# Kernel tuning notes

Measured on AMD Instinct MI355X. Metric: run time of the kernel, lower is better.

Reference implementation:

```python
import jax, jax.numpy as jnp
import numpy as np

N_QUBITS = 24          # must be divisible by 3
DIM = 2 ** N_QUBITS    # 16777216 amplitudes
N_GROUPS = N_QUBITS // 3  # 8 disjoint 3-qubit gate applications


def setup_inputs() -> dict:
    key = jax.random.key(0)
    k1, k2, k3 = jax.random.split(key, 3)
    feature = jax.random.normal(k1, (DIM,), dtype=jnp.float32)
    # Build a random 8x8 unitary as expm of an anti-Hermitian generator,
    # mirroring equivar_gate_matrix = expm(generator) in the original.
    m = (jax.random.normal(k2, (8, 8), dtype=jnp.float32)
         + 1j * jax.random.normal(k3, (8, 8), dtype=jnp.float32)).astype(jnp.complex64)
    gen = 0.5 * (m - m.conj().T)
    gate = jax.scipy.linalg.expm(gen)
    return {
        "feature": feature,
        "gate_real": jnp.real(gate).astype(jnp.float32),
        "gate_imag": jnp.imag(gate).astype(jnp.float32),
    }


def _apply_3q_gate(state, gate, axis):
    # state: (8,)*N_GROUPS complex tensor; contract gate (8x8) into `axis`.
    out = jnp.tensordot(gate, state, axes=[[1], [axis]])  # contracted axis -> front
    return jnp.moveaxis(out, 0, axis)


def reference(feature, gate_real, gate_imag):
    # AmplitudeEmbedding: L2-normalize the feature vector into the state.
    norm = jnp.sqrt(jnp.sum(feature * feature))
    state = (feature / norm).astype(jnp.complex64)
    # View the 24 qubits as 8 groups of 3 (each group = one axis of size 8).
    state = state.reshape((8,) * N_GROUPS)
    gate = (gate_real + 1j * gate_imag).astype(jnp.complex64)
    # QubitUnitary(equivar_gate_matrix, wires=(3i, 3i+1, 3i+2)) for each group.
    for g in range(N_GROUPS):
        state = _apply_3q_gate(state, gate, g)
    # qml.probs(): |amplitude|^2 over the full computational basis.
    probs = (jnp.real(state) ** 2 + jnp.imag(state) ** 2).reshape(-1)
    return probs.astype(jnp.float32)
```

## Files before the change

### kernel.cpp

```cpp
#include <hip/hip_runtime.h>


typedef _Float16 f16;
typedef _Float16 f16x4 __attribute__((ext_vector_type(4)));
typedef float f32x4 __attribute__((ext_vector_type(4)));
typedef unsigned int u32;
typedef unsigned short u16;

__device__ __forceinline__ u32 SW(u32 a) { return a ^ (((a >> 8) & 0xFu) << 3); }

__device__ __forceinline__ u32 PK(float x, float y) {
  return __builtin_bit_cast(u32, __builtin_amdgcn_cvt_pkrtz(x, y));
}

__device__ __forceinline__ f16x4 build_A(const float* __restrict__ gr,
                                         const float* __restrict__ gi, int l) {
  const int row = l & 15, kg = l >> 4;
  const int pg = row & 7, rpl = row >> 3, kpl = kg >> 1;
  f16x4 a;
#pragma unroll
  for (int e = 0; e < 4; ++e) {
    const int j = (kg & 1) * 4 + e;
    const float grv = gr[pg * 8 + j], giv = gi[pg * 8 + j];
    const float v = rpl == 0 ? (kpl == 0 ? grv : -giv) : (kpl == 0 ? giv : grv);
    a[e] = (f16)v;
  }
  return a;
}

__device__ __forceinline__ void lds_stage(char* lb, f16x4 A, int w, int l) {
  const int kg = l >> 4, c = l & 15, c3 = c >> 3, p = kg >> 1;
  const u32 rb = (u32)(w * 512 + c * 32 + kg * 8);
  const f32x4 Z = {0.f, 0.f, 0.f, 0.f};
  f32x4 acc[16];
#pragma unroll
  for (int g = 0; g < 4; ++g) {
#pragma unroll
    for (int m = 0; m < 4; ++m) {
      const int j = (g & 1) + m * 2 + (g >> 1) * 8;
      const uint2 bw = *(const uint2*)(lb + SW(rb + (u32)j * 8192u));
      acc[g * 4 + m] = __builtin_amdgcn_mfma_f32_16x16x16f16(
          A, __builtin_bit_cast(f16x4, bw), Z, 0, 0, 0);
    }
  }
  __syncthreads();
  const u32 wl = (u32)(((w >> 2) << 14) + (((w & 3) * 2 + c3) << 11) +
                       ((c & 7) << 8) + ((kg & 1) << 7) + (p << 4));
#pragma unroll
  for (int g = 0; g < 4; ++g) {
#pragma unroll
    for (int rr = 0; rr < 4; ++rr) {
      const u32 d0 = PK(acc[g * 4 + 0][rr], acc[g * 4 + 1][rr]);
      const u32 d1 = PK(acc[g * 4 + 2][rr], acc[g * 4 + 3][rr]);
      const u32 lg = wl + (u32)(((g & 1) << 16) + ((g >> 1) << 3) + (rr << 5));
      *(uint2*)(lb + SW(lg)) = make_uint2(d0, d1);
    }
  }
  __syncthreads();
}

__global__ __launch_bounds__(1024, 4) void k_pass1(
    const float* __restrict__ f, const float* __restrict__ gr,
    const float* __restrict__ gi, uint4* __restrict__ st,
    float* __restrict__ wsp) {
  __shared__ __align__(16) char lb[131072];
  __shared__ float red[16];
  const int t = threadIdx.x, l = t & 63, w = t >> 6, blk = blockIdx.x;
  const int kg = l >> 4, c = l & 15, c3 = c >> 3, p = kg >> 1;
  const f16x4 A = build_A(gr, gi, l);

  float s = 0.f;
  const float4* fin = (const float4*)f + (size_t)blk * 8192;
  const u32 fl = (u32)(((t >> 7) << 14) + (((t >> 4) & 7) << 11) +
                       (((t >> 1) & 7) << 8) + ((t & 1) << 7));
#pragma unroll
  for (int g2 = 0; g2 < 2; ++g2) {
    float4 v0 = fin[(g2 * 4 + 0) * 1024 + t];
    float4 v1 = fin[(g2 * 4 + 1) * 1024 + t];
    float4 v2 = fin[(g2 * 4 + 2) * 1024 + t];
    float4 v3 = fin[(g2 * 4 + 3) * 1024 + t];
    s += v0.x * v0.x + v0.y * v0.y + v0.z * v0.z + v0.w * v0.w;
    s += v1.x * v1.x + v1.y * v1.y + v1.z * v1.z + v1.w * v1.w;
    s += v2.x * v2.x + v2.y * v2.y + v2.z * v2.z + v2.w * v2.w;
    s += v3.x * v3.x + v3.y * v3.y + v3.z * v3.z + v3.w * v3.w;
#pragma unroll
    for (int q = 0; q < 4; ++q) {
      const float a0 = q == 0 ? v0.x : q == 1 ? v0.y : q == 2 ? v0.z : v0.w;
      const float a1 = q == 0 ? v1.x : q == 1 ? v1.y : q == 2 ? v1.z : v1.w;
      const float a2 = q == 0 ? v2.x : q == 1 ? v2.y : q == 2 ? v2.z : v2.w;
      const float a3 = q == 0 ? v3.x : q == 1 ? v3.y : q == 2 ? v3.z : v3.w;
      const u32 lg = fl + (u32)((q << 5) + (g2 << 3));
      *(uint2*)(lb + SW(lg)) = make_uint2(PK(a0, a1), PK(a2, a3));
      *(uint2*)(lb + SW(lg + 16u)) = make_uint2(0u, 0u);
    }
  }
#pragma unroll
  for (int off = 32; off; off >>= 1) s += __shfl_down(s, off, 64);
  if (l == 0) red[w] = s;
  __syncthreads();
  if (t == 0) {
    float a = 0.f;
#pragma unroll
    for (int i = 0; i < 16; ++i) a += red[i];
    wsp[blk] = a;
  }

  lds_stage(lb, A, w, l);
  lds_stage(lb, A, w, l);
  lds_stage(lb, A, w, l);
  lds_stage(lb, A, w, l);

  const u32 rb = (u32)(w * 512 + c * 32 + kg * 8);
  const f32x4 Z = {0.f, 0.f, 0.f, 0.f};
  const size_t ob = (size_t)blk * 8192;
#pragma unroll
  for (int j = 0; j < 16; ++j) {
    const uint2 bw = *(const uint2*)(lb + SW(rb + (u32)j * 8192u));
    const f32x4 a = __builtin_amdgcn_mfma_f32_16x16x16f16(
        A, __builtin_bit_cast(f16x4, bw), Z, 0, 0, 0);
    const u32 h01 = PK(a[0], a[1]), h23 = PK(a[2], a[3]);
    const u32 q01 = __shfl_xor(h01, 32, 64), q23 = __shfl_xor(h23, 32, 64);
    if (p == 0) {
      const int A3 = j >> 1, A4 = (j & 1) * 4 + (w >> 2), A5 = (w & 3) * 2 + c3;
      uint4 vv;
      vv.x = (h01 & 0xffffu) | (q01 << 16);
      vv.y = (h01 >> 16) | (q01 & 0xffff0000u);
      vv.z = (h23 & 0xffffu) | (q23 << 16);
      vv.w = (h23 >> 16) | (q23 & 0xffff0000u);
      st[ob + (u32)(((A3 * 64 + A4 * 8 + A5) << 4) + ((c & 7) << 1) + (kg & 1))] = vv;
    }
  }
}

__global__ __launch_bounds__(1024, 4) void k_pass2(
    const uint4* gp, const float* __restrict__ gr, const float* __restrict__ gi,
    const float* __restrict__ wsp, float* out) {
  __shared__ __align__(16) char lb[131072];
  __shared__ float red[16];
  const int t = threadIdx.x, l = t & 63, w = t >> 6, b = blockIdx.x;
  const int kg = l >> 4, c = l & 15, c3 = c >> 3, p = kg >> 1;
  const f16x4 A = build_A(gr, gi, l);

  float sp = (t < 512) ? wsp[t] : 0.f;
#pragma unroll
  for (int off = 32; off; off >>= 1) sp += __shfl_down(sp, off, 64);
  if (l == 0) red[w] = sp;

  const u32 fl = (u32)(((t >> 7) << 14) + (((t >> 1) & 7) << 8) +
                       ((t & 1) << 7) + (((t >> 4) & 7) << 1));
#pragma unroll
  for (int it = 0; it < 8; ++it) {
    const uint4 raw = gp[(size_t)(it * 64 + (t >> 4)) * 8192 + (u32)(b * 16 + (t & 15))];
    const u32 lgb = fl + (u32)(it << 11);
#pragma unroll
    for (int dq = 0; dq < 4; ++dq) {
      const u32 dw = dq == 0 ? raw.x : dq == 1 ? raw.y : dq == 2 ? raw.z : raw.w;
      const u32 lg = lgb + (u32)(dq << 5);
      *(u16*)(lb + SW(lg)) = (u16)(dw & 0xffffu);
      *(u16*)(lb + SW(lg + 16u)) = (u16)(dw >> 16);
    }
  }
  __syncthreads();
  float inv;
  {
    float a = 0.f;
#pragma unroll
    for (int i = 0; i < 16; ++i) a += red[i];
    inv = 1.0f / a;
  }

  lds_stage(lb, A, w, l);
  lds_stage(lb, A, w, l);

  const u32 l3 = (u32)((c3 << 14) + ((c & 7) << 11) + ((w & 7) << 5) + (kg << 3));
  const f32x4 Z = {0.f, 0.f, 0.f, 0.f};
#pragma unroll
  for (int j = 0; j < 16; ++j) {
    const u32 jp = (u32)(((j >> 2) << 15) + ((j & 3) << 8) + ((w >> 3) << 10));
    const uint2 bw = *(const uint2*)(lb + SW(l3 + jp));
    const f32x4 a = __builtin_amdgcn_mfma_f32_16x16x16f16(
        A, __builtin_bit_cast(f16x4, bw), Z, 0, 0, 0);
    const int A1 = w & 7, A2 = (w >> 3) * 4 + (j & 3);
    const int A6 = (j >> 2) * 2 + c3, A7 = c & 7;
    const size_t gb = ((size_t)A1 << 18) + ((size_t)A2 << 15) +
                      (u32)(b * 64 + A6 * 8 + A7);
#pragma unroll
    for (int rr = 0; rr < 4; ++rr) {
      float qv = a[rr] * a[rr];
      qv += __shfl_xor(qv, 32, 64);
      if ((rr >> 1) == p) {
        out[gb + ((size_t)((kg & 1) * 4 + rr) << 21)] = qv * inv;
      }
    }
  }
}

extern "C" void kernel_launch(void* const* d_in, const int* in_sizes, int n_in,
                              void* d_out, int out_size, void* d_ws,
                              size_t ws_size, hipStream_t stream) {
  (void)in_sizes; (void)n_in; (void)out_size; (void)ws_size;
  const float* f = (const float*)d_in[0];
  const float* gr = (const float*)d_in[1];
  const float* gi = (const float*)d_in[2];
  float* wsp = (float*)d_ws;

  k_pass1<<<dim3(512), dim3(1024), 0, stream>>>(f, gr, gi, (uint4*)d_out, wsp);
  k_pass2<<<dim3(512), dim3(1024), 0, stream>>>((const uint4*)d_out, gr, gi,
                                                wsp, (float*)d_out);
}
```

Measured before the change: 71.36 us.

## Fuse first gate stage into global load and shrink pass2 blocks

Pass1 now loads the input amplitudes straight from global memory into MFMA B operands, applying the first gate contraction in registers. This drops one LDS staging round trip, so only three LDS stages remain instead of four. Pass2 is restructured into 256-thread blocks with 32KB of LDS, a new swizzle and a new data layout, and the grid grows to 2048 blocks to raise occupancy and overlap. The trade-off is scalar, strided global loads in pass1 in place of float4 loads, which may reduce coalescing.

```diff
diff --git a/kernel.cpp b/kernel.cpp
--- a/kernel.cpp
+++ b/kernel.cpp
@@ -7,7 +7,8 @@
 typedef unsigned int u32;
 typedef unsigned short u16;
 
-__device__ __forceinline__ u32 SW(u32 a) { return a ^ (((a >> 8) & 0xFu) << 3); }
+__device__ __forceinline__ u32 SW1(u32 a) { return a ^ (((a >> 8) & 0xFu) << 3); }
+__device__ __forceinline__ u32 SW2(u32 a) { return a ^ (((a >> 7) & 0x7u) << 4); }
 
 __device__ __forceinline__ u32 PK(float x, float y) {
   return __builtin_bit_cast(u32, __builtin_amdgcn_cvt_pkrtz(x, y));
@@ -28,7 +29,7 @@
   return a;
 }
 
-__device__ __forceinline__ void lds_stage(char* lb, f16x4 A, int w, int l) {
+__device__ __forceinline__ void p1_stage(char* lb, f16x4 A, int w, int l) {
   const int kg = l >> 4, c = l & 15, c3 = c >> 3, p = kg >> 1;
   const u32 rb = (u32)(w * 512 + c * 32 + kg * 8);
   const f32x4 Z = {0.f, 0.f, 0.f, 0.f};
@@ -38,7 +39,7 @@
 #pragma unroll
     for (int m = 0; m < 4; ++m) {
       const int j = (g & 1) + m * 2 + (g >> 1) * 8;
-      const uint2 bw = *(const uint2*)(lb + SW(rb + (u32)j * 8192u));
+      const uint2 bw = *(const uint2*)(lb + SW1(rb + (u32)j * 8192u));
       acc[g * 4 + m] = __builtin_amdgcn_mfma_f32_16x16x16f16(
           A, __builtin_bit_cast(f16x4, bw), Z, 0, 0, 0);
     }
@@ -53,7 +54,7 @@
       const u32 d0 = PK(acc[g * 4 + 0][rr], acc[g * 4 + 1][rr]);
       const u32 d1 = PK(acc[g * 4 + 2][rr], acc[g * 4 + 3][rr]);
       const u32 lg = wl + (u32)(((g & 1) << 16) + ((g >> 1) << 3) + (rr << 5));
-      *(uint2*)(lb + SW(lg)) = make_uint2(d0, d1);
+      *(uint2*)(lb + SW1(lg)) = make_uint2(d0, d1);
     }
   }
   __syncthreads();
@@ -68,30 +69,42 @@
   const int t = threadIdx.x, l = t & 63, w = t >> 6, blk = blockIdx.x;
   const int kg = l >> 4, c = l & 15, c3 = c >> 3, p = kg >> 1;
   const f16x4 A = build_A(gr, gi, l);
+  const f32x4 Z = {0.f, 0.f, 0.f, 0.f};
 
   float s = 0.f;
-  const float4* fin = (const float4*)f + (size_t)blk * 8192;
-  const u32 fl = (u32)(((t >> 7) << 14) + (((t >> 4) & 7) << 11) +
-                       (((t >> 1) & 7) << 8) + ((t & 1) << 7));
-#pragma unroll
-  for (int g2 = 0; g2 < 2; ++g2) {
-    float4 v0 = fin[(g2 * 4 + 0) * 1024 + t];
-    float4 v1 = fin[(g2 * 4 + 1) * 1024 + t];
-    float4 v2 = fin[(g2 * 4 + 2) * 1024 + t];
-    float4 v3 = fin[(g2 * 4 + 3) * 1024 + t];
-    s += v0.x * v0.x + v0.y * v0.y + v0.z * v0.z + v0.w * v0.w;
-    s += v1.x * v1.x + v1.y * v1.y + v1.z * v1.z + v1.w * v1.w;
-    s += v2.x * v2.x + v2.y * v2.y + v2.z * v2.z + v2.w * v2.w;
-    s += v3.x * v3.x + v3.y * v3.y + v3.z * v3.z + v3.w * v3.w;
-#pragma unroll
-    for (int q = 0; q < 4; ++q) {
-      const float a0 = q == 0 ? v0.x : q == 1 ? v0.y : q == 2 ? v0.z : v0.w;
-      const float a1 = q == 0 ? v1.x : q == 1 ? v1.y : q == 2 ? v1.z : v1.w;
-      const float a2 = q == 0 ? v2.x : q == 1 ? v2.y : q == 2 ? v2.z : v2.w;
-      const float a3 = q == 0 ? v3.x : q == 1 ? v3.y : q == 2 ? v3.z : v3.w;
-      const u32 lg = fl + (u32)((q << 5) + (g2 << 3));
-      *(uint2*)(lb + SW(lg)) = make_uint2(PK(a0, a1), PK(a2, a3));
-      *(uint2*)(lb + SW(lg + 16u)) = make_uint2(0u, 0u);
+  {
+    const float* fb = f + ((size_t)blk << 15) + (size_t)(kg & 1) * 16384;
+    f32x4 acc[16];
+#pragma unroll
+    for (int g = 0; g < 4; ++g) {
+#pragma unroll
+      for (int m = 0; m < 4; ++m) {
+        const int j = (g & 1) + m * 2 + (g >> 1) * 8;
+        const int col = (j >> 1) * 512 + (j & 1) * 256 + (w >> 2) * 64 +
+                        (w & 3) * 16 + c;
+        f16x4 b = {(f16)0.f, (f16)0.f, (f16)0.f, (f16)0.f};
+        if (kg < 2) {
+          const float v0 = fb[col];
+          const float v1 = fb[col + 4096];
+          const float v2 = fb[col + 8192];
+          const float v3 = fb[col + 12288];
+          s += v0 * v0 + v1 * v1 + v2 * v2 + v3 * v3;
+          b[0] = (f16)v0; b[1] = (f16)v1; b[2] = (f16)v2; b[3] = (f16)v3;
+        }
+        acc[g * 4 + m] = __builtin_amdgcn_mfma_f32_16x16x16f16(A, b, Z, 0, 0, 0);
+      }
+    }
+    const u32 wl = (u32)(((w >> 2) << 14) + (((w & 3) * 2 + c3) << 11) +
+                         ((c & 7) << 8) + ((kg & 1) << 7) + (p << 4));
+#pragma unroll
+    for (int g = 0; g < 4; ++g) {
+#pragma unroll
+      for (int rr = 0; rr < 4; ++rr) {
+        const u32 d0 = PK(acc[g * 4 + 0][rr], acc[g * 4 + 1][rr]);
+        const u32 d1 = PK(acc[g * 4 + 2][rr], acc[g * 4 + 3][rr]);
+        const u32 lg = wl + (u32)(((g & 1) << 16) + ((g >> 1) << 3) + (rr << 5));
+        *(uint2*)(lb + SW1(lg)) = make_uint2(d0, d1);
+      }
     }
   }
 #pragma unroll
@@ -105,17 +118,15 @@
     wsp[blk] = a;
   }
 
-  lds_stage(lb, A, w, l);
-  lds_stage(lb, A, w, l);
-  lds_stage(lb, A, w, l);
-  lds_stage(lb, A, w, l);
+  p1_stage(lb, A, w, l);
+  p1_stage(lb, A, w, l);
+  p1_stage(lb, A, w, l);
 
   const u32 rb = (u32)(w * 512 + c * 32 + kg * 8);
-  const f32x4 Z = {0.f, 0.f, 0.f, 0.f};
   const size_t ob = (size_t)blk * 8192;
 #pragma unroll
   for (int j = 0; j < 16; ++j) {
-    const uint2 bw = *(const uint2*)(lb + SW(rb + (u32)j * 8192u));
+    const uint2 bw = *(const uint2*)(lb + SW1(rb + (u32)j * 8192u));
     const f32x4 a = __builtin_amdgcn_mfma_f32_16x16x16f16(
         A, __builtin_bit_cast(f16x4, bw), Z, 0, 0, 0);
     const u32 h01 = PK(a[0], a[1]), h23 = PK(a[2], a[3]);
@@ -132,64 +143,101 @@
   }
 }
 
-__global__ __launch_bounds__(1024, 4) void k_pass2(
+__device__ __forceinline__ void p2_stage(char* lb, f16x4 A, int w, int l) {
+  const int kg = l >> 4, c = l & 15, pp = kg >> 1;
+  const f32x4 Z = {0.f, 0.f, 0.f, 0.f};
+  f32x4 acc[16];
+#pragma unroll
+  for (int g = 0; g < 4; ++g) {
+#pragma unroll
+    for (int m = 0; m < 4; ++m) {
+      const int j = (g & 1) + m * 2 + (g >> 1) * 8;
+      const u32 rb = (u32)(j * 2048 + w * 512 + c * 32 + kg * 8);
+      const uint2 bw = *(const uint2*)(lb + SW2(rb));
+      acc[g * 4 + m] = __builtin_amdgcn_mfma_f32_16x16x16f16(
+          A, __builtin_bit_cast(f16x4, bw), Z, 0, 0, 0);
+    }
+  }
+  __syncthreads();
+#pragma unroll
+  for (int pe = 0; pe < 2; ++pe) {
+#pragma unroll
+    for (int rr = 0; rr < 4; ++rr) {
+      uint4 vv;
+      vv.x = PK(acc[pe * 4 + 0][rr], acc[pe * 4 + 1][rr]);
+      vv.y = PK(acc[pe * 4 + 2][rr], acc[pe * 4 + 3][rr]);
+      vv.z = PK(acc[(2 + pe) * 4 + 0][rr], acc[(2 + pe) * 4 + 1][rr]);
+      vv.w = PK(acc[(2 + pe) * 4 + 2][rr], acc[(2 + pe) * 4 + 3][rr]);
+      const u32 wb = (u32)((pe * 4 + w) * 4096 + ((kg & 1) * 4 + rr) * 512 +
+                           c * 32 + pp * 16);
+      *(uint4*)(lb + SW2(wb)) = vv;
+    }
+  }
+  __syncthreads();
+}
+
+__global__ __launch_bounds__(256, 4) void k_pass2(
     const uint4* gp, const float* __restrict__ gr, const float* __restrict__ gi,
     const float* __restrict__ wsp, float* out) {
-  __shared__ __align__(16) char lb[131072];
-  __shared__ float red[16];
-  const int t = threadIdx.x, l = t & 63, w = t >> 6, b = blockIdx.x;
-  const int kg = l >> 4, c = l & 15, c3 = c >> 3, p = kg >> 1;
+  __shared__ __align__(16) char lb[32768];
+  __shared__ float red[4];
+  const int t = threadIdx.x, l = t & 63, w = t >> 6;
+  const int kg = l >> 4, c = l & 15, pp = kg >> 1;
+  const int b9 = blockIdx.x >> 2, q = blockIdx.x & 3;
   const f16x4 A = build_A(gr, gi, l);
-
-  float sp = (t < 512) ? wsp[t] : 0.f;
-#pragma unroll
-  for (int off = 32; off; off >>= 1) sp += __shfl_down(sp, off, 64);
-  if (l == 0) red[w] = sp;
-
-  const u32 fl = (u32)(((t >> 7) << 14) + (((t >> 1) & 7) << 8) +
-                       ((t & 1) << 7) + (((t >> 4) & 7) << 1));
-#pragma unroll
-  for (int it = 0; it < 8; ++it) {
-    const uint4 raw = gp[(size_t)(it * 64 + (t >> 4)) * 8192 + (u32)(b * 16 + (t & 15))];
-    const u32 lgb = fl + (u32)(it << 11);
-#pragma unroll
-    for (int dq = 0; dq < 4; ++dq) {
-      const u32 dw = dq == 0 ? raw.x : dq == 1 ? raw.y : dq == 2 ? raw.z : raw.w;
-      const u32 lg = lgb + (u32)(dq << 5);
-      *(u16*)(lb + SW(lg)) = (u16)(dw & 0xffffu);
-      *(u16*)(lb + SW(lg + 16u)) = (u16)(dw >> 16);
-    }
-  }
-  __syncthreads();
-  float inv;
+  const f32x4 Z = {0.f, 0.f, 0.f, 0.f};
+
+  float sp_ = wsp[t] + wsp[t + 256];
+#pragma unroll
+  for (int off = 32; off; off >>= 1) sp_ += __shfl_down(sp_, off, 64);
+  if (l == 0) red[w] = sp_;
+
   {
-    float a = 0.f;
-#pragma unroll
-    for (int i = 0; i < 16; ++i) a += red[i];
-    inv = 1.0f / a;
-  }
-
-  lds_stage(lb, A, w, l);
-  lds_stage(lb, A, w, l);
-
-  const u32 l3 = (u32)((c3 << 14) + ((c & 7) << 11) + ((w & 7) << 5) + (kg << 3));
-  const f32x4 Z = {0.f, 0.f, 0.f, 0.f};
+    const int z = t >> 2, u = t & 3;
+    const int A1 = z & 7, A0 = z >> 3;
+#pragma unroll
+    for (int a2g = 0; a2g < 2; ++a2g) {
+      uint4 raw[4];
+#pragma unroll
+      for (int d = 0; d < 4; ++d)
+        raw[d] = gp[(size_t)(z * 8 + 4 * a2g + d) * 8192 + (u32)(b9 * 16 + q * 4 + u)];
+#pragma unroll
+      for (int v = 0; v < 4; ++v) {
+        const u32 w0 = v == 0 ? raw[0].x : v == 1 ? raw[0].y : v == 2 ? raw[0].z : raw[0].w;
+        const u32 w1 = v == 0 ? raw[1].x : v == 1 ? raw[1].y : v == 2 ? raw[1].z : raw[1].w;
+        const u32 w2 = v == 0 ? raw[2].x : v == 1 ? raw[2].y : v == 2 ? raw[2].z : raw[2].w;
+        const u32 w3 = v == 0 ? raw[3].x : v == 1 ? raw[3].y : v == 2 ? raw[3].z : raw[3].w;
+        const int sp = u * 4 + v;
+        const u32 base = (u32)(A1 * 4096 + A0 * 512 + sp * 32 + 8 * a2g);
+        *(uint2*)(lb + SW2(base)) =
+            make_uint2((w0 & 0xffffu) | (w1 << 16), (w2 & 0xffffu) | (w3 << 16));
+        *(uint2*)(lb + SW2(base + 16u)) =
+            make_uint2((w0 >> 16) | (w1 & 0xffff0000u), (w2 >> 16) | (w3 & 0xffff0000u));
+      }
+    }
+  }
+  __syncthreads();
+  const float inv = 1.0f / (red[0] + red[1] + red[2] + red[3]);
+
+  p2_stage(lb, A, w, l);
+  p2_stage(lb, A, w, l);
+
 #pragma unroll
   for (int j = 0; j < 16; ++j) {
-    const u32 jp = (u32)(((j >> 2) << 15) + ((j & 3) << 8) + ((w >> 3) << 10));
-    const uint2 bw = *(const uint2*)(lb + SW(l3 + jp));
+    const u32 rb = (u32)(j * 2048 + w * 512 + c * 32 + kg * 8);
+    const uint2 bw = *(const uint2*)(lb + SW2(rb));
     const f32x4 a = __builtin_amdgcn_mfma_f32_16x16x16f16(
         A, __builtin_bit_cast(f16x4, bw), Z, 0, 0, 0);
-    const int A1 = w & 7, A2 = (w >> 3) * 4 + (j & 3);
-    const int A6 = (j >> 2) * 2 + c3, A7 = c & 7;
+    const int A2 = j >> 1, A1 = (j & 1) * 4 + w;
     const size_t gb = ((size_t)A1 << 18) + ((size_t)A2 << 15) +
-                      (u32)(b * 64 + A6 * 8 + A7);
+                      (u32)(b9 * 64 + q * 16 + c);
 #pragma unroll
     for (int rr = 0; rr < 4; ++rr) {
       float qv = a[rr] * a[rr];
       qv += __shfl_xor(qv, 32, 64);
-      if ((rr >> 1) == p) {
-        out[gb + ((size_t)((kg & 1) * 4 + rr) << 21)] = qv * inv;
+      if ((rr >> 1) == pp) {
+        const size_t A0 = (size_t)((kg & 1) * 4 + rr);
+        out[gb + (A0 << 21)] = qv * inv;
       }
     }
   }
@@ -205,6 +253,6 @@
   float* wsp = (float*)d_ws;
 
   k_pass1<<<dim3(512), dim3(1024), 0, stream>>>(f, gr, gi, (uint4*)d_out, wsp);
-  k_pass2<<<dim3(512), dim3(1024), 0, stream>>>((const uint4*)d_out, gr, gi,
+  k_pass2<<<dim3(2048), dim3(256), 0, stream>>>((const uint4*)d_out, gr, gi,
                                                 wsp, (float*)d_out);
 }
```

After: 77.75 us. 8.9% more time.

## Rebalance gate passes into 4+4 split with smaller blocks and separate norm kernel

Applied to the files above, without the earlier changes.

Changes the split of the eight 3-qubit contractions from 5 in pass1 and 3 in pass2 to 4 and 4. Pass1 now uses 256-thread blocks with 16KB LDS across 4096 blocks, and pass2 uses 512-thread blocks with 64KB LDS across 1024 blocks, to raise occupancy and cut LDS footprint. The first pass1 stage skips the zero-padded imaginary half, and the global-to-LDS repacking is rewritten with new layouts. A tiny single-block k_norm kernel now reduces the norm partials, which adds an extra launch and serialization point.

```diff
diff --git a/kernel.cpp b/kernel.cpp
--- a/kernel.cpp
+++ b/kernel.cpp
@@ -5,9 +5,8 @@
 typedef _Float16 f16x4 __attribute__((ext_vector_type(4)));
 typedef float f32x4 __attribute__((ext_vector_type(4)));
 typedef unsigned int u32;
-typedef unsigned short u16;
-
-__device__ __forceinline__ u32 SW(u32 a) { return a ^ (((a >> 8) & 0xFu) << 3); }
+
+__device__ __forceinline__ u32 SWZ(u32 a) { return a ^ (((a >> 8) & 0xFu) << 3); }
 
 __device__ __forceinline__ u32 PK(float x, float y) {
   return __builtin_bit_cast(u32, __builtin_amdgcn_cvt_pkrtz(x, y));
@@ -28,170 +27,208 @@
   return a;
 }
 
-__device__ __forceinline__ void lds_stage(char* lb, f16x4 A, int w, int l) {
-  const int kg = l >> 4, c = l & 15, c3 = c >> 3, p = kg >> 1;
-  const u32 rb = (u32)(w * 512 + c * 32 + kg * 8);
-  const f32x4 Z = {0.f, 0.f, 0.f, 0.f};
-  f32x4 acc[16];
-#pragma unroll
-  for (int g = 0; g < 4; ++g) {
-#pragma unroll
-    for (int m = 0; m < 4; ++m) {
-      const int j = (g & 1) + m * 2 + (g >> 1) * 8;
-      const uint2 bw = *(const uint2*)(lb + SW(rb + (u32)j * 8192u));
-      acc[g * 4 + m] = __builtin_amdgcn_mfma_f32_16x16x16f16(
-          A, __builtin_bit_cast(f16x4, bw), Z, 0, 0, 0);
-    }
-  }
-  __syncthreads();
-  const u32 wl = (u32)(((w >> 2) << 14) + (((w & 3) * 2 + c3) << 11) +
-                       ((c & 7) << 8) + ((kg & 1) << 7) + (p << 4));
-#pragma unroll
-  for (int g = 0; g < 4; ++g) {
+__device__ __forceinline__ f32x4 MF(f16x4 A, uint2 bw, f32x4 C) {
+  return __builtin_amdgcn_mfma_f32_16x16x16f16(A, __builtin_bit_cast(f16x4, bw),
+                                               C, 0, 0, 0);
+}
+
+template <bool FIRST>
+__device__ __forceinline__ void p1_stage(char* lb, f16x4 A, int w, int l) {
+  const int kg = l >> 4, c = l & 15, c3 = c >> 3, kg0 = kg & 1, kg1 = kg >> 1;
+  const f32x4 Z = {0.f, 0.f, 0.f, 0.f};
+  const u32 rbase = (u32)((((w << 1) | c3) << 8) | ((c & 7) << 5) | (kg1 << 4) |
+                          (kg0 << 3));
+  f32x4 acc[8];
+#pragma unroll
+  for (int j = 0; j < 8; ++j) {
+    uint2 bw = make_uint2(0u, 0u);
+    if (!FIRST || kg < 2)
+      bw = *(const uint2*)(lb + SWZ(rbase + ((u32)j << 11)));
+    acc[j] = MF(A, bw, Z);
+  }
+  __syncthreads();
+  const u32 wbase = (u32)(((((w << 1) | c3)) << 11) | ((c & 7) << 8) |
+                          (kg1 << 4));
+#pragma unroll
+  for (int q = 0; q < 2; ++q) {
 #pragma unroll
     for (int rr = 0; rr < 4; ++rr) {
-      const u32 d0 = PK(acc[g * 4 + 0][rr], acc[g * 4 + 1][rr]);
-      const u32 d1 = PK(acc[g * 4 + 2][rr], acc[g * 4 + 3][rr]);
-      const u32 lg = wl + (u32)(((g & 1) << 16) + ((g >> 1) << 3) + (rr << 5));
-      *(uint2*)(lb + SW(lg)) = make_uint2(d0, d1);
-    }
-  }
-  __syncthreads();
-}
-
-__global__ __launch_bounds__(1024, 4) void k_pass1(
+      const u32 d0 = PK(acc[4 * q + 0][rr], acc[4 * q + 1][rr]);
+      const u32 d1 = PK(acc[4 * q + 2][rr], acc[4 * q + 3][rr]);
+      const u32 lg = wbase + (u32)(((kg0 * 4 + rr) << 5) | (q << 3));
+      *(uint2*)(lb + SWZ(lg)) = make_uint2(d0, d1);
+    }
+  }
+  __syncthreads();
+}
+
+__global__ __launch_bounds__(256, 4) void k_pass1(
     const float* __restrict__ f, const float* __restrict__ gr,
-    const float* __restrict__ gi, uint4* __restrict__ st,
+    const float* __restrict__ gi, u32* __restrict__ st,
     float* __restrict__ wsp) {
-  __shared__ __align__(16) char lb[131072];
-  __shared__ float red[16];
-  const int t = threadIdx.x, l = t & 63, w = t >> 6, blk = blockIdx.x;
-  const int kg = l >> 4, c = l & 15, c3 = c >> 3, p = kg >> 1;
+  __shared__ __align__(16) char lb[16384];
+  __shared__ float red[4];
+  const int t = threadIdx.x, l = t & 63, w = t >> 6, b = blockIdx.x;
+  const int kg = l >> 4, c = l & 15, c3 = c >> 3, kg0 = kg & 1, kg1 = kg >> 1;
   const f16x4 A = build_A(gr, gi, l);
-
-  float s = 0.f;
-  const float4* fin = (const float4*)f + (size_t)blk * 8192;
-  const u32 fl = (u32)(((t >> 7) << 14) + (((t >> 4) & 7) << 11) +
-                       (((t >> 1) & 7) << 8) + ((t & 1) << 7));
-#pragma unroll
-  for (int g2 = 0; g2 < 2; ++g2) {
-    float4 v0 = fin[(g2 * 4 + 0) * 1024 + t];
-    float4 v1 = fin[(g2 * 4 + 1) * 1024 + t];
-    float4 v2 = fin[(g2 * 4 + 2) * 1024 + t];
-    float4 v3 = fin[(g2 * 4 + 3) * 1024 + t];
-    s += v0.x * v0.x + v0.y * v0.y + v0.z * v0.z + v0.w * v0.w;
-    s += v1.x * v1.x + v1.y * v1.y + v1.z * v1.z + v1.w * v1.w;
-    s += v2.x * v2.x + v2.y * v2.y + v2.z * v2.z + v2.w * v2.w;
-    s += v3.x * v3.x + v3.y * v3.y + v3.z * v3.z + v3.w * v3.w;
-#pragma unroll
-    for (int q = 0; q < 4; ++q) {
-      const float a0 = q == 0 ? v0.x : q == 1 ? v0.y : q == 2 ? v0.z : v0.w;
-      const float a1 = q == 0 ? v1.x : q == 1 ? v1.y : q == 2 ? v1.z : v1.w;
-      const float a2 = q == 0 ? v2.x : q == 1 ? v2.y : q == 2 ? v2.z : v2.w;
-      const float a3 = q == 0 ? v3.x : q == 1 ? v3.y : q == 2 ? v3.z : v3.w;
-      const u32 lg = fl + (u32)((q << 5) + (g2 << 3));
-      *(uint2*)(lb + SW(lg)) = make_uint2(PK(a0, a1), PK(a2, a3));
-      *(uint2*)(lb + SW(lg + 16u)) = make_uint2(0u, 0u);
-    }
-  }
-#pragma unroll
-  for (int off = 32; off; off >>= 1) s += __shfl_down(s, off, 64);
-  if (l == 0) red[w] = s;
-  __syncthreads();
-  if (t == 0) {
-    float a = 0.f;
-#pragma unroll
-    for (int i = 0; i < 16; ++i) a += red[i];
-    wsp[blk] = a;
-  }
-
-  lds_stage(lb, A, w, l);
-  lds_stage(lb, A, w, l);
-  lds_stage(lb, A, w, l);
-  lds_stage(lb, A, w, l);
-
-  const u32 rb = (u32)(w * 512 + c * 32 + kg * 8);
-  const f32x4 Z = {0.f, 0.f, 0.f, 0.f};
-  const size_t ob = (size_t)blk * 8192;
-#pragma unroll
-  for (int j = 0; j < 16; ++j) {
-    const uint2 bw = *(const uint2*)(lb + SW(rb + (u32)j * 8192u));
-    const f32x4 a = __builtin_amdgcn_mfma_f32_16x16x16f16(
-        A, __builtin_bit_cast(f16x4, bw), Z, 0, 0, 0);
+  const f32x4 Z = {0.f, 0.f, 0.f, 0.f};
+
+  {
+    const float* fb = f + ((size_t)b << 12);
+    float v[16];
+#pragma unroll
+    for (int u = 0; u < 2; ++u) {
+      const int low9 = u * 256 + t;
+#pragma unroll
+      for (int a4 = 0; a4 < 8; ++a4) v[u * 8 + a4] = fb[a4 * 512 + low9];
+    }
+    float s = 0.f;
+#pragma unroll
+    for (int i = 0; i < 16; ++i) s += v[i] * v[i];
+#pragma unroll
+    for (int u = 0; u < 2; ++u) {
+      const int low9 = u * 256 + t;
+      const int A5 = low9 >> 6, A6 = (low9 >> 3) & 7, A7 = low9 & 7;
+      const u32 bb = (u32)((A5 << 11) | (A6 << 8) | (A7 << 5));
+      *(uint2*)(lb + SWZ(bb)) =
+          make_uint2(PK(v[u * 8 + 0], v[u * 8 + 1]), PK(v[u * 8 + 2], v[u * 8 + 3]));
+      *(uint2*)(lb + SWZ(bb | 8u)) =
+          make_uint2(PK(v[u * 8 + 4], v[u * 8 + 5]), PK(v[u * 8 + 6], v[u * 8 + 7]));
+    }
+#pragma unroll
+    for (int off = 32; off; off >>= 1) s += __shfl_down(s, off, 64);
+    if (l == 0) red[w] = s;
+  }
+  __syncthreads();
+  if (t == 0) wsp[b] = (red[0] + red[1]) + (red[2] + red[3]);
+
+  p1_stage<true>(lb, A, w, l);
+  p1_stage<false>(lb, A, w, l);
+  p1_stage<false>(lb, A, w, l);
+
+  const u32 rbase = (u32)((((w << 1) | c3) << 8) | ((c & 7) << 5) | (kg1 << 4) |
+                          (kg0 << 3));
+  const u32 ob = (u32)b << 12;
+#pragma unroll
+  for (int j = 0; j < 8; ++j) {
+    const uint2 bw = *(const uint2*)(lb + SWZ(rbase + ((u32)j << 11)));
+    const f32x4 a = MF(A, bw, Z);
     const u32 h01 = PK(a[0], a[1]), h23 = PK(a[2], a[3]);
     const u32 q01 = __shfl_xor(h01, 32, 64), q23 = __shfl_xor(h23, 32, 64);
-    if (p == 0) {
-      const int A3 = j >> 1, A4 = (j & 1) * 4 + (w >> 2), A5 = (w & 3) * 2 + c3;
-      uint4 vv;
-      vv.x = (h01 & 0xffffu) | (q01 << 16);
-      vv.y = (h01 >> 16) | (q01 & 0xffff0000u);
-      vv.z = (h23 & 0xffffu) | (q23 << 16);
-      vv.w = (h23 >> 16) | (q23 & 0xffff0000u);
-      st[ob + (u32)(((A3 * 64 + A4 * 8 + A5) << 4) + ((c & 7) << 1) + (kg & 1))] = vv;
-    }
-  }
-}
-
-__global__ __launch_bounds__(1024, 4) void k_pass2(
-    const uint4* gp, const float* __restrict__ gr, const float* __restrict__ gi,
-    const float* __restrict__ wsp, float* out) {
-  __shared__ __align__(16) char lb[131072];
-  __shared__ float red[16];
-  const int t = threadIdx.x, l = t & 63, w = t >> 6, b = blockIdx.x;
-  const int kg = l >> 4, c = l & 15, c3 = c >> 3, p = kg >> 1;
+    const u32 d0 = kg1 ? ((q23 & 0xffffu) | (h23 << 16))
+                       : ((h01 & 0xffffu) | (q01 << 16));
+    const u32 d1 = kg1 ? ((q23 >> 16) | (h23 & 0xffff0000u))
+                       : ((h01 >> 16) | (q01 & 0xffff0000u));
+    const u32 low12 = (u32)((j << 9) | (((w << 1) | c3) << 6) | ((c & 7) << 3) |
+                            (kg0 * 4 + 2 * kg1));
+    *(uint2*)(st + ob + low12) = make_uint2(d0, d1);
+  }
+}
+
+__global__ __launch_bounds__(256) void k_norm(float* __restrict__ wsp) {
+  const int t = threadIdx.x;
+  float s = 0.f;
+#pragma unroll
+  for (int i = 0; i < 16; ++i) s += wsp[i * 256 + t];
+#pragma unroll
+  for (int off = 32; off; off >>= 1) s += __shfl_down(s, off, 64);
+  __shared__ float red[4];
+  if ((t & 63) == 0) red[t >> 6] = s;
+  __syncthreads();
+  if (t == 0) wsp[4096] = 1.0f / ((red[0] + red[1]) + (red[2] + red[3]));
+}
+
+__device__ __forceinline__ void p2_stage(char* lb, f16x4 A, int w, int l) {
+  const int kg = l >> 4, c = l & 15, kg0 = kg & 1, kg1 = kg >> 1;
+  const int spc = c & 3, c2b = c >> 2;
+  const f32x4 Z = {0.f, 0.f, 0.f, 0.f};
+  f32x4 acc[16];
+#pragma unroll
+  for (int j = 0; j < 16; ++j) {
+    const u32 rb = (u32)(((j >> 1) << 13) | (((((j & 1) << 2) | (w >> 1))) << 10) |
+                         (spc << 8) | (((((w & 1) << 2) | c2b)) << 5) |
+                         (kg1 << 4) | (kg0 << 3));
+    acc[j] = MF(A, *(const uint2*)(lb + SWZ(rb)), Z);
+  }
+  __syncthreads();
+  const u32 wb0 = (u32)((((((w & 1) << 2) | c2b)) << 10) | (spc << 8) | (kg1 << 4));
+#pragma unroll
+  for (int jp = 0; jp < 4; ++jp) {
+    const int j0 = (jp & 1) | ((jp >> 1) << 3);
+#pragma unroll
+    for (int rr = 0; rr < 4; ++rr) {
+      const u32 d0 = PK(acc[j0][rr], acc[j0 + 2][rr]);
+      const u32 d1 = PK(acc[j0 + 4][rr], acc[j0 + 6][rr]);
+      const u32 lg = wb0 + (u32)(((((j0 & 1) << 2) | (w >> 1)) << 13) |
+                                 ((kg0 * 4 + rr) << 5) | ((j0 >> 3) << 3));
+      *(uint2*)(lb + SWZ(lg)) = make_uint2(d0, d1);
+    }
+  }
+  __syncthreads();
+}
+
+__global__ __launch_bounds__(512, 4) void k_pass2(
+    const uint4* __restrict__ gp, const float* __restrict__ gr,
+    const float* __restrict__ gi, const float* __restrict__ invp,
+    float* __restrict__ out) {
+  __shared__ __align__(16) char lb[65536];
+  const int t = threadIdx.x, l = t & 63, w = t >> 6;
+  const int kg = l >> 4, c = l & 15, kg0 = kg & 1, kg1 = kg >> 1;
+  const int spc = c & 3, c2b = c >> 2;
+  const int bid = blockIdx.x;
+  const int Lb = (bid & 7) * 128 + (bid >> 3);
   const f16x4 A = build_A(gr, gi, l);
-
-  float sp = (t < 512) ? wsp[t] : 0.f;
-#pragma unroll
-  for (int off = 32; off; off >>= 1) sp += __shfl_down(sp, off, 64);
-  if (l == 0) red[w] = sp;
-
-  const u32 fl = (u32)(((t >> 7) << 14) + (((t >> 1) & 7) << 8) +
-                       ((t & 1) << 7) + (((t >> 4) & 7) << 1));
-#pragma unroll
-  for (int it = 0; it < 8; ++it) {
-    const uint4 raw = gp[(size_t)(it * 64 + (t >> 4)) * 8192 + (u32)(b * 16 + (t & 15))];
-    const u32 lgb = fl + (u32)(it << 11);
-#pragma unroll
-    for (int dq = 0; dq < 4; ++dq) {
-      const u32 dw = dq == 0 ? raw.x : dq == 1 ? raw.y : dq == 2 ? raw.z : raw.w;
-      const u32 lg = lgb + (u32)(dq << 5);
-      *(u16*)(lb + SW(lg)) = (u16)(dw & 0xffffu);
-      *(u16*)(lb + SW(lg + 16u)) = (u16)(dw >> 16);
-    }
-  }
-  __syncthreads();
-  float inv;
+  const f32x4 Z = {0.f, 0.f, 0.f, 0.f};
+
   {
-    float a = 0.f;
-#pragma unroll
-    for (int i = 0; i < 16; ++i) a += red[i];
-    inv = 1.0f / a;
-  }
-
-  lds_stage(lb, A, w, l);
-  lds_stage(lb, A, w, l);
-
-  const u32 l3 = (u32)((c3 << 14) + ((c & 7) << 11) + ((w & 7) << 5) + (kg << 3));
-  const f32x4 Z = {0.f, 0.f, 0.f, 0.f};
+    uint4 r8[8];
+#pragma unroll
+    for (int a0 = 0; a0 < 8; ++a0)
+      r8[a0] = gp[(size_t)(a0 * 512 + t) * 1024 + (u32)Lb];
+    const int A1 = t >> 6, A2 = (t >> 3) & 7, A3 = t & 7;
+    const u32 fb = (u32)((A1 << 13) | (A2 << 10) | (A3 << 5));
+#pragma unroll
+    for (int sp = 0; sp < 4; ++sp) {
+      u32 dv[8];
+#pragma unroll
+      for (int a0 = 0; a0 < 8; ++a0) {
+        const uint4 r = r8[a0];
+        dv[a0] = sp == 0 ? r.x : sp == 1 ? r.y : sp == 2 ? r.z : r.w;
+      }
+      const u32 bb = fb + (u32)(sp << 8);
+      *(uint2*)(lb + SWZ(bb)) =
+          make_uint2((dv[0] & 0xffffu) | (dv[1] << 16), (dv[2] & 0xffffu) | (dv[3] << 16));
+      *(uint2*)(lb + SWZ(bb | 8u)) =
+          make_uint2((dv[4] & 0xffffu) | (dv[5] << 16), (dv[6] & 0xffffu) | (dv[7] << 16));
+      *(uint2*)(lb + SWZ(bb | 16u)) =
+          make_uint2((dv[0] >> 16) | (dv[1] & 0xffff0000u), (dv[2] >> 16) | (dv[3] & 0xffff0000u));
+      *(uint2*)(lb + SWZ(bb | 24u)) =
+          make_uint2((dv[4] >> 16) | (dv[5] & 0xffff0000u), (dv[6] >> 16) | (dv[7] & 0xffff0000u));
+    }
+  }
+  __syncthreads();
+  const float inv = invp[0];
+
+  p2_stage(lb, A, w, l);
+  p2_stage(lb, A, w, l);
+  p2_stage(lb, A, w, l);
+
 #pragma unroll
   for (int j = 0; j < 16; ++j) {
-    const u32 jp = (u32)(((j >> 2) << 15) + ((j & 3) << 8) + ((w >> 3) << 10));
-    const uint2 bw = *(const uint2*)(lb + SW(l3 + jp));
-    const f32x4 a = __builtin_amdgcn_mfma_f32_16x16x16f16(
-        A, __builtin_bit_cast(f16x4, bw), Z, 0, 0, 0);
-    const int A1 = w & 7, A2 = (w >> 3) * 4 + (j & 3);
-    const int A6 = (j >> 2) * 2 + c3, A7 = c & 7;
-    const size_t gb = ((size_t)A1 << 18) + ((size_t)A2 << 15) +
-                      (u32)(b * 64 + A6 * 8 + A7);
-#pragma unroll
-    for (int rr = 0; rr < 4; ++rr) {
-      float qv = a[rr] * a[rr];
-      qv += __shfl_xor(qv, 32, 64);
-      if ((rr >> 1) == p) {
-        out[gb + ((size_t)((kg & 1) * 4 + rr) << 21)] = qv * inv;
-      }
-    }
+    const u32 rb = (u32)(((j >> 1) << 13) | (((((j & 1) << 2) | (w >> 1))) << 10) |
+                         (spc << 8) | (((((w & 1) << 2) | c2b)) << 5) |
+                         (kg1 << 4) | (kg0 << 3));
+    const f32x4 a = MF(A, *(const uint2*)(lb + SWZ(rb)), Z);
+    float qv0 = a[0] * a[0]; qv0 += __shfl_xor(qv0, 32, 64);
+    float qv1 = a[1] * a[1]; qv1 += __shfl_xor(qv1, 32, 64);
+    float qv2 = a[2] * a[2]; qv2 += __shfl_xor(qv2, 32, 64);
+    float qv3 = a[3] * a[3]; qv3 += __shfl_xor(qv3, 32, 64);
+    const u32 hib = (u32)(((j >> 1) << 9) | ((((j & 1) << 2) | (w >> 1)) << 6) |
+                          ((((w & 1) << 2) | c2b) << 3));
+    const u32 a3b = (u32)(kg0 * 4 + 2 * kg1);
+    const size_t n0 = ((size_t)(hib + a3b) << 12) + (u32)(Lb * 4 + spc);
+    out[n0] = (kg1 ? qv2 : qv0) * inv;
+    out[n0 + 4096] = (kg1 ? qv3 : qv1) * inv;
   }
 }
 
@@ -204,7 +241,8 @@
   const float* gi = (const float*)d_in[2];
   float* wsp = (float*)d_ws;
 
-  k_pass1<<<dim3(512), dim3(1024), 0, stream>>>(f, gr, gi, (uint4*)d_out, wsp);
-  k_pass2<<<dim3(512), dim3(1024), 0, stream>>>((const uint4*)d_out, gr, gi,
-                                                wsp, (float*)d_out);
-}
+  k_pass1<<<dim3(4096), dim3(256), 0, stream>>>(f, gr, gi, (u32*)d_out, wsp);
+  k_norm<<<dim3(1), dim3(256), 0, stream>>>(wsp);
+  k_pass2<<<dim3(1024), dim3(512), 0, stream>>>((const uint4*)d_out, gr, gi,
+                                                wsp + 4096, (float*)d_out);
+}
```

After: 72.64 us. Within noise of the previous version (+1.8%).
